# Performance work log

Hardware: AMD Instinct MI355X
Metric: run time of the kernel (lower is better)

Reference implementation:

```python
import jax, jax.numpy as jnp
import numpy as np

N, NFEAT, NHID, NCLASS, NLAYERS = 10000, 512, 256, 40, 8
LAMDA, ALPHA = 0.5, 0.1
EDGE_P = 0.003  # avg degree ~30


def setup_inputs() -> dict:
    key = jax.random.key(0)
    ks = jax.random.split(key, 8)
    x = jax.random.normal(ks[0], (N, NFEAT), dtype=jnp.float32)
    # binary adjacency with zero diagonal (normalize_adj asserts diag==0)
    adj = (jax.random.uniform(ks[1], (N, N)) < EDGE_P).astype(jnp.float32)
    adj = adj * (1.0 - jnp.eye(N, dtype=jnp.float32))
    # GraphConvolution.reset_parameters: uniform(-1/sqrt(out), 1/sqrt(out))
    s = 1.0 / np.sqrt(NHID)
    conv_w = jax.random.uniform(ks[2], (NLAYERS, NHID, NHID), jnp.float32, -s, s)
    s0 = 1.0 / np.sqrt(NFEAT)
    w0 = jax.random.uniform(ks[3], (NFEAT, NHID), jnp.float32, -s0, s0)
    b0 = jax.random.uniform(ks[4], (NHID,), jnp.float32, -s0, s0)
    s1 = 1.0 / np.sqrt(NHID)
    w1 = jax.random.uniform(ks[5], (NHID, NCLASS), jnp.float32, -s1, s1)
    b1 = jax.random.uniform(ks[6], (NCLASS,), jnp.float32, -s1, s1)
    return {"x": x, "adj": adj, "w0": w0, "b0": b0, "conv_w": conv_w, "w1": w1, "b1": b1}


def reference(x, adj, w0, b0, conv_w, w1, b1):
    n = adj.shape[0]
    # normalize_adj: A_hat = A + I; D^{-1/2} A_hat D^{-1/2}
    a_hat = adj + jnp.eye(n, dtype=adj.dtype)
    d_inv_sqrt = jax.lax.rsqrt(jnp.sum(a_hat, axis=1))
    a_norm = a_hat * d_inv_sqrt[:, None] * d_inv_sqrt[None, :]

    # dropout is a no-op in eval mode
    h0 = jax.nn.relu(x @ w0 + b0)  # [N, NHID]
    thetas = jnp.log(LAMDA / jnp.arange(1, NLAYERS + 1, dtype=jnp.float32) + 1.0)

    def step(h, wt):
        w, theta = wt
        hi = a_norm @ h                              # aggregation
        support = (1.0 - ALPHA) * hi + ALPHA * h0    # initial-residual mix (variant=False: r = support)
        out = theta * (support @ w) + (1.0 - theta) * support
        return jax.nn.relu(out), None

    h, _ = jax.lax.scan(step, h0, (conv_w, thetas))
    logits = h @ w1 + b1  # [N, NCLASS]
    return jax.nn.log_softmax(logits, axis=1)
```

## Files before the change

### kernel.cpp

```cpp
#include <hip/hip_runtime.h>
#include <math.h>

#define NN 10000
#define NFEAT 512
#define NHID 256
#define NCLASS 40
#define NLAYERS 8
#define MAXDEG 96

typedef __attribute__((ext_vector_type(8))) short bf16x8;
typedef __attribute__((ext_vector_type(4))) float floatx4;
typedef __attribute__((ext_vector_type(4))) unsigned short ushort4v;

__device__ __forceinline__ unsigned short f2bf(float f) {
    union { float f; unsigned int u; } v; v.f = f;
    unsigned int r = v.u + 0x7fffu + ((v.u >> 16) & 1u);
    return (unsigned short)(r >> 16);
}
__device__ __forceinline__ float bf2f(unsigned short h) {
    union { unsigned int u; float f; } v; v.u = ((unsigned int)h) << 16;
    return v.f;
}

__global__ __launch_bounds__(256) void build_graph(const float* __restrict__ adj,
                                                   int* __restrict__ cnt,
                                                   int* __restrict__ ell,
                                                   float* __restrict__ dinv) {
    int i = blockIdx.x;
    __shared__ int scnt;
    if (threadIdx.x == 0) scnt = 0;
    __syncthreads();
    const float4* row = (const float4*)(adj + (size_t)i * NN);
    const int nv = NN / 4;
    int* erow = ell + (size_t)i * MAXDEG;
    for (int f = threadIdx.x; f < nv; f += 256) {
        float4 v = row[f];
        if (v.x != 0.0f) { int s = atomicAdd(&scnt, 1); if (s < MAXDEG) erow[s] = 4*f + 0; }
        if (v.y != 0.0f) { int s = atomicAdd(&scnt, 1); if (s < MAXDEG) erow[s] = 4*f + 1; }
        if (v.z != 0.0f) { int s = atomicAdd(&scnt, 1); if (s < MAXDEG) erow[s] = 4*f + 2; }
        if (v.w != 0.0f) { int s = atomicAdd(&scnt, 1); if (s < MAXDEG) erow[s] = 4*f + 3; }
    }
    __syncthreads();
    if (threadIdx.x == 0) {
        int c = scnt;
        cnt[i] = (c < MAXDEG) ? c : MAXDEG;
        dinv[i] = rsqrtf(1.0f + (float)c);
    }
}

__global__ __launch_bounds__(256) void convert_x(const float* __restrict__ x,
                                                 unsigned short* __restrict__ xb) {
    int idx = blockIdx.x * 256 + threadIdx.x;
    float4 v = ((const float4*)x)[idx];
    ushort4v o;
    o.x = f2bf(v.x); o.y = f2bf(v.y); o.z = f2bf(v.z); o.w = f2bf(v.w);
    ((ushort4v*)xb)[idx] = o;
}

__global__ __launch_bounds__(256) void prep_weights(const float* __restrict__ w0,
                                                    const float* __restrict__ cw,
                                                    unsigned short* __restrict__ w0t,
                                                    unsigned short* __restrict__ cwt) {
    int idx = blockIdx.x * 256 + threadIdx.x;
    if (idx < 131072) {
        int n = idx >> 9, k = idx & 511;
        w0t[idx] = f2bf(w0[(size_t)k * 256 + n]);
    } else {
        int j = idx - 131072;
        int l = j >> 16;
        int r = j & 65535;
        int n = r >> 8, k = r & 255;
        cwt[j] = f2bf(cw[(size_t)l * 65536 + (size_t)k * 256 + n]);
    }
}

__global__ __launch_bounds__(256) void gemm0_mfma(const unsigned short* __restrict__ xb,
                                                  const unsigned short* __restrict__ w0t,
                                                  const float* __restrict__ b0,
                                                  float* __restrict__ h0f,
                                                  unsigned short* __restrict__ h0b) {
    int t = threadIdx.x, wv = t >> 6, lane = t & 63;
    int lrow = lane & 15, quad = lane >> 4;
    int r0 = blockIdx.x * 16;

    bf16x8 a[16];
    const unsigned short* arow = xb + (size_t)(r0 + lrow) * NFEAT + quad * 8;
    #pragma unroll
    for (int f = 0; f < 16; ++f)
        a[f] = *(const bf16x8*)(arow + f * 32);

    #pragma unroll 1
    for (int n = 0; n < 4; ++n) {
        int nt = wv * 4 + n;
        floatx4 acc = {0.f, 0.f, 0.f, 0.f};
        const unsigned short* wrow = w0t + (size_t)(nt * 16 + lrow) * NFEAT + quad * 8;
        #pragma unroll
        for (int f = 0; f < 16; ++f) {
            bf16x8 b = *(const bf16x8*)(wrow + f * 32);
            acc = __builtin_amdgcn_mfma_f32_16x16x32_bf16(a[f], b, acc, 0, 0, 0);
        }
        int col = nt * 16 + lrow;
        float bias = b0[col];
        #pragma unroll
        for (int r = 0; r < 4; ++r) {
            int row = r0 + quad * 4 + r;
            float o = fmaxf(acc[r] + bias, 0.f);
            h0f[(size_t)row * NHID + col] = o;
            h0b[(size_t)row * NHID + col] = f2bf(o);
        }
    }
}

template<bool LAST>
__global__ __launch_bounds__(256) void layer_fused(const unsigned short* __restrict__ hb,
                                                   const float* __restrict__ h0f,
                                                   const float* __restrict__ dinv,
                                                   const int* __restrict__ cnt,
                                                   const int* __restrict__ ell,
                                                   const unsigned short* __restrict__ Wt,
                                                   float theta,
                                                   unsigned short* __restrict__ hb_out,
                                                   float* __restrict__ hf_out) {
    __shared__ float          supf[16][264];
    __shared__ unsigned short supb[16][264];
    __shared__ int   sj[16][MAXDEG];
    __shared__ float scl[16][MAXDEG];

    int t = threadIdx.x, wv = t >> 6, lane = t & 63;
    int r0 = blockIdx.x * 16;

    #pragma unroll
    for (int rr = 0; rr < 4; ++rr) {
        int lr = wv * 4 + rr;
        int i  = r0 + lr;
        int deg = cnt[i];
        for (int e = lane; e < deg; e += 64) {
            int j = ell[(size_t)i * MAXDEG + e];
            sj[lr][e]  = j;
            scl[lr][e] = dinv[j];
        }
    }
    __syncthreads();

    const ushort4v* hv = (const ushort4v*)hb;
    #pragma unroll 1
    for (int rr = 0; rr < 4; ++rr) {
        int lr = wv * 4 + rr;
        int i  = r0 + lr;
        int deg = cnt[i];
        float di = dinv[i];
        ushort4v sv = hv[(size_t)i * 64 + lane];
        float4 acc;
        acc.x = di * bf2f(sv.x);
        acc.y = di * bf2f(sv.y);
        acc.z = di * bf2f(sv.z);
        acc.w = di * bf2f(sv.w);
        #pragma unroll 4
        for (int e = 0; e < deg; ++e) {
            float s = scl[lr][e];
            ushort4v xv = hv[(size_t)sj[lr][e] * 64 + lane];
            acc.x = fmaf(s, bf2f(xv.x), acc.x);
            acc.y = fmaf(s, bf2f(xv.y), acc.y);
            acc.z = fmaf(s, bf2f(xv.z), acc.z);
            acc.w = fmaf(s, bf2f(xv.w), acc.w);
        }
        float4 h0v = ((const float4*)h0f)[(size_t)i * 64 + lane];
        float4 o;
        o.x = 0.9f * (di * acc.x) + 0.1f * h0v.x;
        o.y = 0.9f * (di * acc.y) + 0.1f * h0v.y;
        o.z = 0.9f * (di * acc.z) + 0.1f * h0v.z;
        o.w = 0.9f * (di * acc.w) + 0.1f * h0v.w;
        *(float4*)&supf[lr][4 * lane] = o;
        ushort4v ob;
        ob.x = f2bf(o.x); ob.y = f2bf(o.y); ob.z = f2bf(o.z); ob.w = f2bf(o.w);
        *(ushort4v*)&supb[lr][4 * lane] = ob;
    }
    __syncthreads();

    int lrow = lane & 15, quad = lane >> 4;
    bf16x8 a[8];
    #pragma unroll
    for (int f = 0; f < 8; ++f)
        a[f] = *(const bf16x8*)&supb[lrow][quad * 8 + f * 32];

    float om = 1.0f - theta;
    #pragma unroll 1
    for (int n = 0; n < 4; ++n) {
        int nt = wv * 4 + n;
        floatx4 acc = {0.f, 0.f, 0.f, 0.f};
        const unsigned short* wrow = Wt + (size_t)(nt * 16 + lrow) * NHID + quad * 8;
        #pragma unroll
        for (int f = 0; f < 8; ++f) {
            bf16x8 b = *(const bf16x8*)(wrow + f * 32);
            acc = __builtin_amdgcn_mfma_f32_16x16x32_bf16(a[f], b, acc, 0, 0, 0);
        }
        int col = nt * 16 + lrow;
        #pragma unroll
        for (int r = 0; r < 4; ++r) {
            int lr2 = quad * 4 + r;
            int row = r0 + lr2;
            float s = supf[lr2][col];
            float o = fmaxf(fmaf(theta, acc[r], om * s), 0.f);
            hb_out[(size_t)row * NHID + col] = f2bf(o);
            if (LAST) hf_out[(size_t)row * NHID + col] = o;
        }
    }
}

__global__ __launch_bounds__(256) void final_logits(const float* __restrict__ h,
                                                    const float* __restrict__ w1,
                                                    const float* __restrict__ b1,
                                                    float* __restrict__ out) {
    __shared__ float hs[4 * NHID];
    int r0 = blockIdx.x * 4;
    ((float4*)hs)[threadIdx.x] = ((const float4*)(h + (size_t)r0 * NHID))[threadIdx.x];
    __syncthreads();
    int row  = threadIdx.x >> 6;
    int lane = threadIdx.x & 63;
    const float* hr = hs + row * NHID;
    float logit = -1e30f;
    if (lane < NCLASS) {
        float acc = b1[lane];
        #pragma unroll 8
        for (int k = 0; k < NHID; ++k)
            acc = fmaf(hr[k], w1[k * NCLASS + lane], acc);
        logit = acc;
    }
    float m = logit;
    #pragma unroll
    for (int off = 32; off > 0; off >>= 1)
        m = fmaxf(m, __shfl_xor(m, off, 64));
    float e = (lane < NCLASS) ? expf(logit - m) : 0.0f;
    float ssum = e;
    #pragma unroll
    for (int off = 32; off > 0; off >>= 1)
        ssum += __shfl_xor(ssum, off, 64);
    float lse = m + logf(ssum);
    if (lane < NCLASS)
        out[(size_t)(r0 + row) * NCLASS + lane] = logit - lse;
}

extern "C" void kernel_launch(void* const* d_in, const int* in_sizes, int n_in,
                              void* d_out, int out_size, void* d_ws, size_t ws_size,
                              hipStream_t stream) {
    const float* x      = (const float*)d_in[0];
    const float* adj    = (const float*)d_in[1];
    const float* w0     = (const float*)d_in[2];
    const float* b0     = (const float*)d_in[3];
    const float* conv_w = (const float*)d_in[4];
    const float* w1     = (const float*)d_in[5];
    const float* b1     = (const float*)d_in[6];
    float* out = (float*)d_out;

    char* ws = (char*)d_ws;
    size_t off = 0;
    auto alloc = [&](size_t bytes) -> void* {
        void* p = ws + off;
        off = (off + bytes + 255) & ~(size_t)255;
        return p;
    };
    float*          dinv = (float*)alloc((size_t)NN * 4);
    int*            cnt  = (int*)  alloc((size_t)NN * 4);
    int*            ell  = (int*)  alloc((size_t)NN * MAXDEG * 4);
    unsigned short* xb   = (unsigned short*)alloc((size_t)NN * NFEAT * 2);
    unsigned short* w0t  = (unsigned short*)alloc((size_t)NFEAT * NHID * 2);
    unsigned short* cwt  = (unsigned short*)alloc((size_t)NLAYERS * NHID * NHID * 2);
    float*          h0f  = (float*)alloc((size_t)NN * NHID * 4);
    unsigned short* h0b  = (unsigned short*)alloc((size_t)NN * NHID * 2);
    unsigned short* hPb  = (unsigned short*)alloc((size_t)NN * NHID * 2);
    unsigned short* hQb  = (unsigned short*)alloc((size_t)NN * NHID * 2);
    float*          hfL  = (float*)alloc((size_t)NN * NHID * 4);

    build_graph<<<NN, 256, 0, stream>>>(adj, cnt, ell, dinv);
    convert_x<<<(NN * NFEAT / 4) / 256, 256, 0, stream>>>(x, xb);
    prep_weights<<<(131072 + NLAYERS * NHID * NHID) / 256, 256, 0, stream>>>(w0, conv_w, w0t, cwt);

    gemm0_mfma<<<NN / 16, 256, 0, stream>>>(xb, w0t, b0, h0f, h0b);

    const unsigned short* hcb = h0b;
    for (int l = 0; l < NLAYERS; ++l) {
        float theta = logf(0.5f / (float)(l + 1) + 1.0f);
        unsigned short* nxt = (l & 1) ? hQb : hPb;
        const unsigned short* wt = cwt + (size_t)l * NHID * NHID;
        if (l == NLAYERS - 1)
            layer_fused<true><<<NN / 16, 256, 0, stream>>>(hcb, h0f, dinv, cnt, ell, wt, theta, nxt, hfL);
        else
            layer_fused<false><<<NN / 16, 256, 0, stream>>>(hcb, h0f, dinv, cnt, ell, wt, theta, nxt, nullptr);
        hcb = nxt;
    }
    final_logits<<<NN / 4, 256, 0, stream>>>(hfL, w1, b1, out);
}
```

Measured before the change: 886.1 us.

## Fold theta residual into weight matrix, drop fp32 h0, fuse logits into last layer

Folds theta*W + (1-theta)*I into one bf16 matrix per layer during weight prep, so the epilogue becomes a plain ReLU and the fp32 support tile in shared memory goes away. The fp32 copy of h0 is removed and the residual mix reads the bf16 h0 instead, halving that read. The separate final_logits kernel is fused into the last layer, which computes logits and log-softmax from a shared-memory tile, so the fp32 final hidden state is never written to global memory. The trade is more bf16 rounding, since the identity term is now quantised into the matrix and h0 is bf16, plus a serial per-wave logits loop and extra shared memory in the last layer.

```diff
diff --git a/kernel.cpp b/kernel.cpp
--- a/kernel.cpp
+++ b/kernel.cpp
@@ -60,7 +60,7 @@
 __global__ __launch_bounds__(256) void prep_weights(const float* __restrict__ w0,
                                                     const float* __restrict__ cw,
                                                     unsigned short* __restrict__ w0t,
-                                                    unsigned short* __restrict__ cwt) {
+                                                    unsigned short* __restrict__ Mt) {
     int idx = blockIdx.x * 256 + threadIdx.x;
     if (idx < 131072) {
         int n = idx >> 9, k = idx & 511;
@@ -70,14 +70,16 @@
         int l = j >> 16;
         int r = j & 65535;
         int n = r >> 8, k = r & 255;
-        cwt[j] = f2bf(cw[(size_t)l * 65536 + (size_t)k * 256 + n]);
+        float theta = logf(0.5f / (float)(l + 1) + 1.0f);
+        float v = theta * cw[(size_t)l * 65536 + (size_t)k * 256 + n];
+        if (k == n) v += 1.0f - theta;
+        Mt[j] = f2bf(v);
     }
 }
 
 __global__ __launch_bounds__(256) void gemm0_mfma(const unsigned short* __restrict__ xb,
                                                   const unsigned short* __restrict__ w0t,
                                                   const float* __restrict__ b0,
-                                                  float* __restrict__ h0f,
                                                   unsigned short* __restrict__ h0b) {
     int t = threadIdx.x, wv = t >> 6, lane = t & 63;
     int lrow = lane & 15, quad = lane >> 4;
@@ -104,27 +106,26 @@
         #pragma unroll
         for (int r = 0; r < 4; ++r) {
             int row = r0 + quad * 4 + r;
-            float o = fmaxf(acc[r] + bias, 0.f);
-            h0f[(size_t)row * NHID + col] = o;
-            h0b[(size_t)row * NHID + col] = f2bf(o);
+            h0b[(size_t)row * NHID + col] = f2bf(fmaxf(acc[r] + bias, 0.f));
         }
     }
 }
 
 template<bool LAST>
 __global__ __launch_bounds__(256) void layer_fused(const unsigned short* __restrict__ hb,
-                                                   const float* __restrict__ h0f,
+                                                   const unsigned short* __restrict__ h0b,
                                                    const float* __restrict__ dinv,
                                                    const int* __restrict__ cnt,
                                                    const int* __restrict__ ell,
-                                                   const unsigned short* __restrict__ Wt,
-                                                   float theta,
+                                                   const unsigned short* __restrict__ Mt,
+                                                   const float* __restrict__ w1,
+                                                   const float* __restrict__ b1,
                                                    unsigned short* __restrict__ hb_out,
-                                                   float* __restrict__ hf_out) {
-    __shared__ float          supf[16][264];
+                                                   float* __restrict__ out) {
     __shared__ unsigned short supb[16][264];
     __shared__ int   sj[16][MAXDEG];
     __shared__ float scl[16][MAXDEG];
+    __shared__ float hs[LAST ? 16 * 264 : 4];
 
     int t = threadIdx.x, wv = t >> 6, lane = t & 63;
     int r0 = blockIdx.x * 16;
@@ -164,15 +165,12 @@
             acc.z = fmaf(s, bf2f(xv.z), acc.z);
             acc.w = fmaf(s, bf2f(xv.w), acc.w);
         }
-        float4 h0v = ((const float4*)h0f)[(size_t)i * 64 + lane];
-        float4 o;
-        o.x = 0.9f * (di * acc.x) + 0.1f * h0v.x;
-        o.y = 0.9f * (di * acc.y) + 0.1f * h0v.y;
-        o.z = 0.9f * (di * acc.z) + 0.1f * h0v.z;
-        o.w = 0.9f * (di * acc.w) + 0.1f * h0v.w;
-        *(float4*)&supf[lr][4 * lane] = o;
+        ushort4v h0v = ((const ushort4v*)h0b)[(size_t)i * 64 + lane];
         ushort4v ob;
-        ob.x = f2bf(o.x); ob.y = f2bf(o.y); ob.z = f2bf(o.z); ob.w = f2bf(o.w);
+        ob.x = f2bf(0.9f * (di * acc.x) + 0.1f * bf2f(h0v.x));
+        ob.y = f2bf(0.9f * (di * acc.y) + 0.1f * bf2f(h0v.y));
+        ob.z = f2bf(0.9f * (di * acc.z) + 0.1f * bf2f(h0v.z));
+        ob.w = f2bf(0.9f * (di * acc.w) + 0.1f * bf2f(h0v.w));
         *(ushort4v*)&supb[lr][4 * lane] = ob;
     }
     __syncthreads();
@@ -183,12 +181,11 @@
     for (int f = 0; f < 8; ++f)
         a[f] = *(const bf16x8*)&supb[lrow][quad * 8 + f * 32];
 
-    float om = 1.0f - theta;
     #pragma unroll 1
     for (int n = 0; n < 4; ++n) {
         int nt = wv * 4 + n;
         floatx4 acc = {0.f, 0.f, 0.f, 0.f};
-        const unsigned short* wrow = Wt + (size_t)(nt * 16 + lrow) * NHID + quad * 8;
+        const unsigned short* wrow = Mt + (size_t)(nt * 16 + lrow) * NHID + quad * 8;
         #pragma unroll
         for (int f = 0; f < 8; ++f) {
             bf16x8 b = *(const bf16x8*)(wrow + f * 32);
@@ -198,46 +195,43 @@
         #pragma unroll
         for (int r = 0; r < 4; ++r) {
             int lr2 = quad * 4 + r;
-            int row = r0 + lr2;
-            float s = supf[lr2][col];
-            float o = fmaxf(fmaf(theta, acc[r], om * s), 0.f);
-            hb_out[(size_t)row * NHID + col] = f2bf(o);
-            if (LAST) hf_out[(size_t)row * NHID + col] = o;
-        }
-    }
-}
-
-__global__ __launch_bounds__(256) void final_logits(const float* __restrict__ h,
-                                                    const float* __restrict__ w1,
-                                                    const float* __restrict__ b1,
-                                                    float* __restrict__ out) {
-    __shared__ float hs[4 * NHID];
-    int r0 = blockIdx.x * 4;
-    ((float4*)hs)[threadIdx.x] = ((const float4*)(h + (size_t)r0 * NHID))[threadIdx.x];
-    __syncthreads();
-    int row  = threadIdx.x >> 6;
-    int lane = threadIdx.x & 63;
-    const float* hr = hs + row * NHID;
-    float logit = -1e30f;
-    if (lane < NCLASS) {
-        float acc = b1[lane];
-        #pragma unroll 8
-        for (int k = 0; k < NHID; ++k)
-            acc = fmaf(hr[k], w1[k * NCLASS + lane], acc);
-        logit = acc;
-    }
-    float m = logit;
-    #pragma unroll
-    for (int off = 32; off > 0; off >>= 1)
-        m = fmaxf(m, __shfl_xor(m, off, 64));
-    float e = (lane < NCLASS) ? expf(logit - m) : 0.0f;
-    float ssum = e;
-    #pragma unroll
-    for (int off = 32; off > 0; off >>= 1)
-        ssum += __shfl_xor(ssum, off, 64);
-    float lse = m + logf(ssum);
-    if (lane < NCLASS)
-        out[(size_t)(r0 + row) * NCLASS + lane] = logit - lse;
+            float o = fmaxf(acc[r], 0.f);
+            if (LAST) {
+                hs[lr2 * 264 + col] = o;
+            } else {
+                hb_out[(size_t)(r0 + lr2) * NHID + col] = f2bf(o);
+            }
+        }
+    }
+
+    if (LAST) {
+        __syncthreads();
+        #pragma unroll 1
+        for (int rr = 0; rr < 4; ++rr) {
+            int lr = wv * 4 + rr;
+            const float* hr = hs + lr * 264;
+            float logit = -1e30f;
+            if (lane < NCLASS) {
+                float acc = b1[lane];
+                #pragma unroll 8
+                for (int k = 0; k < NHID; ++k)
+                    acc = fmaf(hr[k], w1[k * NCLASS + lane], acc);
+                logit = acc;
+            }
+            float m = logit;
+            #pragma unroll
+            for (int off = 32; off > 0; off >>= 1)
+                m = fmaxf(m, __shfl_xor(m, off, 64));
+            float e = (lane < NCLASS) ? expf(logit - m) : 0.0f;
+            float ssum = e;
+            #pragma unroll
+            for (int off = 32; off > 0; off >>= 1)
+                ssum += __shfl_xor(ssum, off, 64);
+            float lse = m + logf(ssum);
+            if (lane < NCLASS)
+                out[(size_t)(r0 + lr) * NCLASS + lane] = logit - lse;
+        }
+    }
 }
 
 extern "C" void kernel_launch(void* const* d_in, const int* in_sizes, int n_in,
@@ -264,29 +258,25 @@
     int*            ell  = (int*)  alloc((size_t)NN * MAXDEG * 4);
     unsigned short* xb   = (unsigned short*)alloc((size_t)NN * NFEAT * 2);
     unsigned short* w0t  = (unsigned short*)alloc((size_t)NFEAT * NHID * 2);
-    unsigned short* cwt  = (unsigned short*)alloc((size_t)NLAYERS * NHID * NHID * 2);
-    float*          h0f  = (float*)alloc((size_t)NN * NHID * 4);
+    unsigned short* Mt   = (unsigned short*)alloc((size_t)NLAYERS * NHID * NHID * 2);
     unsigned short* h0b  = (unsigned short*)alloc((size_t)NN * NHID * 2);
     unsigned short* hPb  = (unsigned short*)alloc((size_t)NN * NHID * 2);
     unsigned short* hQb  = (unsigned short*)alloc((size_t)NN * NHID * 2);
-    float*          hfL  = (float*)alloc((size_t)NN * NHID * 4);
 
     build_graph<<<NN, 256, 0, stream>>>(adj, cnt, ell, dinv);
     convert_x<<<(NN * NFEAT / 4) / 256, 256, 0, stream>>>(x, xb);
-    prep_weights<<<(131072 + NLAYERS * NHID * NHID) / 256, 256, 0, stream>>>(w0, conv_w, w0t, cwt);
-
-    gemm0_mfma<<<NN / 16, 256, 0, stream>>>(xb, w0t, b0, h0f, h0b);
+    prep_weights<<<(131072 + NLAYERS * NHID * NHID) / 256, 256, 0, stream>>>(w0, conv_w, w0t, Mt);
+
+    gemm0_mfma<<<NN / 16, 256, 0, stream>>>(xb, w0t, b0, h0b);
 
     const unsigned short* hcb = h0b;
     for (int l = 0; l < NLAYERS; ++l) {
-        float theta = logf(0.5f / (float)(l + 1) + 1.0f);
         unsigned short* nxt = (l & 1) ? hQb : hPb;
-        const unsigned short* wt = cwt + (size_t)l * NHID * NHID;
+        const unsigned short* wt = Mt + (size_t)l * NHID * NHID;
         if (l == NLAYERS - 1)
-            layer_fused<true><<<NN / 16, 256, 0, stream>>>(hcb, h0f, dinv, cnt, ell, wt, theta, nxt, hfL);
+            layer_fused<true><<<NN / 16, 256, 0, stream>>>(hcb, h0b, dinv, cnt, ell, wt, w1, b1, nullptr, out);
         else
-            layer_fused<false><<<NN / 16, 256, 0, stream>>>(hcb, h0f, dinv, cnt, ell, wt, theta, nxt, nullptr);
+            layer_fused<false><<<NN / 16, 256, 0, stream>>>(hcb, h0b, dinv, cnt, ell, wt, nullptr, nullptr, nxt, nullptr);
         hcb = nxt;
     }
-    final_logits<<<NN / 4, 256, 0, stream>>>(hfL, w1, b1, out);
-}
+}
```

After: 880.2 us. Within noise of the previous version (-0.7%).
